# Performance work log

Hardware: AMD Instinct MI355X
Metric: run time of the kernel (lower is better)

The kernel has to match this reference:

```python
import jax, jax.numpy as jnp
import numpy as np

B, S, HID = 2, 2048, 2048
NH = 16
HD = HID // NH  # 128


def setup_inputs() -> dict:
    key = jax.random.key(0)
    ks = jax.random.split(key, 9)
    w = 0.02  # init scale to keep logits in a sane range
    return {
        "hidden_states": jax.random.normal(ks[0], (B, S, HID), dtype=jnp.float32),
        "Wq": jax.random.normal(ks[1], (HID, HID), dtype=jnp.float32) * w,
        "bq": jnp.zeros((HID,), dtype=jnp.float32),
        "Wk": jax.random.normal(ks[2], (HID, HD), dtype=jnp.float32) * w,
        "bk": jnp.zeros((HD,), dtype=jnp.float32),
        "Wv": jax.random.normal(ks[3], (HID, HD), dtype=jnp.float32) * w,
        "bv": jnp.zeros((HD,), dtype=jnp.float32),
        "Wo": jax.random.normal(ks[4], (HID, HID), dtype=jnp.float32) * w,
        "bo": jnp.zeros((HID,), dtype=jnp.float32),
    }


def reference(hidden_states, Wq, bq, Wk, bk, Wv, bv, Wo, bo):
    b, s, _ = hidden_states.shape
    # Projections (weights stored [in, out])
    q = hidden_states @ Wq + bq                      # [B,S,HID]
    k = hidden_states @ Wk + bk                      # [B,S,HD] single shared KV head
    v = hidden_states @ Wv + bv                      # [B,S,HD]
    q = q.reshape(b, s, NH, HD)                      # [B,S,H,D]
    # MQA: all query heads attend to the same K/V
    scores = jnp.einsum("bshd,btd->bhst", q, k) / jnp.sqrt(jnp.float32(HD))  # [B,H,S,S]
    probs = jax.nn.softmax(scores, axis=-1)
    attn = jnp.einsum("bhst,btd->bshd", probs, v)    # [B,S,H,D]
    attn = attn.reshape(b, s, HID)
    return attn @ Wo + bo
```

## Files before the change

### kernel.cpp

```cpp
#include <hip/hip_runtime.h>
#include <math.h>

#define BB  2
#define SS  2048
#define HID 2048
#define NH  16
#define HD  128
#define MT  (BB * SS)
#define NC  (HID + 2 * HD)
#define QK_SCALE 0.08838834764831845f

typedef unsigned short ushort_t;
typedef unsigned int uint_t;
typedef __bf16 bf16x8 __attribute__((ext_vector_type(8)));
typedef short short8 __attribute__((ext_vector_type(8)));
typedef float f32x4 __attribute__((ext_vector_type(4)));

__device__ __forceinline__ ushort_t f2bf(float x) {
    union { float f; uint_t u; } a; a.f = x;
    return (ushort_t)((a.u + 0x7FFFu + ((a.u >> 16) & 1u)) >> 16);
}
__device__ __forceinline__ ushort_t f2bf_fast(float x) {
    union { float f; uint_t u; } a; a.f = x;
    return (ushort_t)((a.u + 0x8000u) >> 16);
}

__device__ __forceinline__ int sw_addr(int r, int c) {
    return ((r >> 1) << 6) + ((((((r & 1) << 2) | c)) ^ ((r >> 1) & 7)) << 3);
}

#define CFENCE() asm volatile("" ::: "memory")

__global__ __launch_bounds__(256) void conv_bf16_kernel(
    const float* __restrict__ in, ushort_t* __restrict__ outb)
{
    const size_t i = ((size_t)blockIdx.x * 256 + threadIdx.x) * 8;
    const float4 a = *(const float4*)&in[i];
    const float4 b = *(const float4*)&in[i + 4];
    short8 o;
    o[0] = (short)f2bf(a.x); o[1] = (short)f2bf(a.y);
    o[2] = (short)f2bf(a.z); o[3] = (short)f2bf(a.w);
    o[4] = (short)f2bf(b.x); o[5] = (short)f2bf(b.y);
    o[6] = (short)f2bf(b.z); o[7] = (short)f2bf(b.w);
    *(short8*)&outb[i] = o;
}

__global__ __launch_bounds__(256) void convT_kernel(
    const float* __restrict__ W, ushort_t* __restrict__ Th, int K, int N)
{
    __shared__ float Ts[64][65];
    const int t = threadIdx.x;
    const int k0 = blockIdx.x * 64, n0 = blockIdx.y * 64;
    const int rr = t >> 4, c4 = (t & 15) * 4;
#pragma unroll
    for (int i = 0; i < 4; i++) {
        const int k = rr + i * 16;
        const float4 v = *(const float4*)&W[(size_t)(k0 + k) * N + n0 + c4];
        Ts[k][c4 + 0] = v.x; Ts[k][c4 + 1] = v.y;
        Ts[k][c4 + 2] = v.z; Ts[k][c4 + 3] = v.w;
    }
    __syncthreads();
    const int n = t >> 2, kc = (t & 3) * 16;
    short8 hv[2];
#pragma unroll
    for (int jj = 0; jj < 16; jj++)
        hv[jj >> 3][jj & 7] = (short)f2bf(Ts[kc + jj][n]);
    const size_t ob = (size_t)(n0 + n) * K + k0 + kc;
    *(short8*)&Th[ob]     = hv[0];
    *(short8*)&Th[ob + 8] = hv[1];
}

__global__ __launch_bounds__(256, 2) void gemm_qkv_kernel(
    const ushort_t* __restrict__ Ab, const ushort_t* __restrict__ WT,
    const float* __restrict__ bq, const float* __restrict__ bk,
    const float* __restrict__ bv,
    ushort_t* __restrict__ qb, ushort_t* __restrict__ kb,
    ushort_t* __restrict__ vtb)
{
    __shared__ short lds[8192];
    constexpr int AH = 0, BH = 4096;
    constexpr int K = HID;
    const int t  = threadIdx.x;
    const int wv = t >> 6, ln = t & 63;
    const int row0 = blockIdx.y * 128, col0 = blockIdx.x * 128;

    size_t agbase[2], bgbase[2];
    int    lbase[2];
#pragma unroll
    for (int i = 0; i < 2; i++) {
        const int I = wv * 2 + i;
        const int lrow = I * 8 + (ln >> 3);
        const int sb = (ln & 7) ^ (lrow & 7);
        const int rr = lrow * 2 + (sb >> 2);
        const int cc = sb & 3;
        agbase[i] = (size_t)(row0 + rr) * K + cc * 8;
        bgbase[i] = (size_t)(col0 + rr) * K + cc * 8;
        lbase[i] = I * 512;
    }

    const int wm0 = (wv & 1) * 64, wn0 = (wv >> 1) * 64;
    const int q = ln >> 4, lm = ln & 15;
    int aoff[4], boff[4];
#pragma unroll
    for (int i = 0; i < 4; i++) aoff[i] = sw_addr(wm0 + i * 16 + lm, q);
#pragma unroll
    for (int j = 0; j < 4; j++) boff[j] = sw_addr(wn0 + j * 16 + lm, q);

    f32x4 acc[4][4];
#pragma unroll
    for (int i = 0; i < 4; i++)
#pragma unroll
        for (int j = 0; j < 4; j++) acc[i][j] = 0.f;

    for (int k0 = 0; k0 < K; k0 += 32) {
        __syncthreads();
#pragma unroll
        for (int i = 0; i < 2; i++) {
            __builtin_amdgcn_global_load_lds(
                (const __attribute__((address_space(1))) void*)(Ab + agbase[i] + k0),
                (__attribute__((address_space(3))) void*)&lds[AH + lbase[i]], 16, 0, 0);
            __builtin_amdgcn_global_load_lds(
                (const __attribute__((address_space(1))) void*)(WT + bgbase[i] + k0),
                (__attribute__((address_space(3))) void*)&lds[BH + lbase[i]], 16, 0, 0);
        }
        __syncthreads();

        bf16x8 ah[4], bh[4];
#pragma unroll
        for (int i = 0; i < 4; i++) ah[i] = *(const bf16x8*)&lds[AH + aoff[i]];
#pragma unroll
        for (int j = 0; j < 4; j++) bh[j] = *(const bf16x8*)&lds[BH + boff[j]];
#pragma unroll
        for (int i = 0; i < 4; i++)
#pragma unroll
            for (int j = 0; j < 4; j++)
                acc[i][j] = __builtin_amdgcn_mfma_f32_16x16x32_bf16(ah[i], bh[j], acc[i][j], 0, 0, 0);
    }

    const int mode = (col0 < HID) ? 0 : ((col0 == HID) ? 1 : 2);
    const float* bsel = (mode == 0) ? bq : ((mode == 1) ? bk : bv);
    const int noff = (mode == 0) ? 0 : ((mode == 1) ? HID : HID + HD);
    float bj[4];
#pragma unroll
    for (int j = 0; j < 4; j++) bj[j] = bsel[col0 - noff + wn0 + j * 16 + lm];
#pragma unroll
    for (int i = 0; i < 4; i++) {
        const int mb = row0 + wm0 + i * 16 + q * 4;
#pragma unroll
        for (int j = 0; j < 4; j++) {
            const int nn = col0 + wn0 + j * 16 + lm;
#pragma unroll
            for (int rr2 = 0; rr2 < 4; rr2++) {
                const float v = acc[i][j][rr2] + bj[j];
                if (mode == 0)      qb [(size_t)(mb + rr2) * HID + nn]           = f2bf_fast(v * QK_SCALE);
                else if (mode == 1) kb [(size_t)(mb + rr2) * HD + (nn - HID)]    = f2bf_fast(v);
                else                vtb[(size_t)(nn - HID - HD) * MT + mb + rr2] = f2bf_fast(v);
            }
        }
    }
}

__global__ __launch_bounds__(256, 2) void gemm_oproj_kernel(
    const ushort_t* __restrict__ Ab, const ushort_t* __restrict__ WT,
    const float* __restrict__ bias, float* __restrict__ C, int M, int N, int K)
{
    __shared__ short lds[8192];
    constexpr int AH = 0, BH = 4096;
    const int t  = threadIdx.x;
    const int wv = t >> 6, ln = t & 63;
    const int row0 = blockIdx.y * 128, col0 = blockIdx.x * 128;

    size_t agbase[2], bgbase[2];
    int    lbase[2];
#pragma unroll
    for (int i = 0; i < 2; i++) {
        const int I = wv * 2 + i;
        const int lrow = I * 8 + (ln >> 3);
        const int sb = (ln & 7) ^ (lrow & 7);
        const int rr = lrow * 2 + (sb >> 2);
        const int cc = sb & 3;
        agbase[i] = (size_t)(row0 + rr) * K + cc * 8;
        bgbase[i] = (size_t)(col0 + rr) * K + cc * 8;
        lbase[i] = I * 512;
    }

    const int wm0 = (wv & 1) * 64, wn0 = (wv >> 1) * 64;
    const int q = ln >> 4, lm = ln & 15;
    int aoff[4], boff[4];
#pragma unroll
    for (int i = 0; i < 4; i++) aoff[i] = sw_addr(wm0 + i * 16 + lm, q);
#pragma unroll
    for (int j = 0; j < 4; j++) boff[j] = sw_addr(wn0 + j * 16 + lm, q);

    f32x4 acc[4][4];
#pragma unroll
    for (int i = 0; i < 4; i++)
#pragma unroll
        for (int j = 0; j < 4; j++) acc[i][j] = 0.f;

    for (int k0 = 0; k0 < K; k0 += 32) {
        __syncthreads();
#pragma unroll
        for (int i = 0; i < 2; i++) {
            __builtin_amdgcn_global_load_lds(
                (const __attribute__((address_space(1))) void*)(Ab + agbase[i] + k0),
                (__attribute__((address_space(3))) void*)&lds[AH + lbase[i]], 16, 0, 0);
            __builtin_amdgcn_global_load_lds(
                (const __attribute__((address_space(1))) void*)(WT + bgbase[i] + k0),
                (__attribute__((address_space(3))) void*)&lds[BH + lbase[i]], 16, 0, 0);
        }
        __syncthreads();

        bf16x8 ah[4], bh[4];
#pragma unroll
        for (int i = 0; i < 4; i++) ah[i] = *(const bf16x8*)&lds[AH + aoff[i]];
#pragma unroll
        for (int j = 0; j < 4; j++) bh[j] = *(const bf16x8*)&lds[BH + boff[j]];
#pragma unroll
        for (int i = 0; i < 4; i++)
#pragma unroll
            for (int j = 0; j < 4; j++)
                acc[i][j] = __builtin_amdgcn_mfma_f32_16x16x32_bf16(ah[i], bh[j], acc[i][j], 0, 0, 0);
    }

    float bj[4];
#pragma unroll
    for (int j = 0; j < 4; j++) bj[j] = bias[col0 + wn0 + j * 16 + lm];
#pragma unroll
    for (int i = 0; i < 4; i++) {
        const int mb = row0 + wm0 + i * 16 + q * 4;
#pragma unroll
        for (int j = 0; j < 4; j++) {
            const int nn = col0 + wn0 + j * 16 + lm;
#pragma unroll
            for (int rr2 = 0; rr2 < 4; rr2++)
                C[(size_t)(mb + rr2) * N + nn] = acc[i][j][rr2] + bj[j];
        }
    }
}

__global__ __launch_bounds__(256, 2) void attn_mfma_kernel(
    const ushort_t* __restrict__ qg, const ushort_t* __restrict__ kg,
    const ushort_t* __restrict__ vtg, ushort_t* Oh)
{
    __shared__ short Ks[2][8192], Vts[2][8192], Ps[4096];
    const int b = blockIdx.z, h = blockIdx.y, qt = blockIdx.x;
    const int t = threadIdx.x, wv = t >> 6, ln = t & 63;
    const int q = ln >> 4, lm = ln & 15;
    const int w16 = wv * 16;
    const int am = w16 + lm, amx = am & 15, amx7 = am & 7;

#pragma unroll
    for (int i = 0; i < 4; i++) {
        const int I = wv * 4 + i;
        const int r = 4 * I + (ln >> 4);
        const int c = (ln & 15) ^ (r & 15);
        const ushort_t* src = qg + (size_t)(b * SS + qt * 64 + r) * HID + h * HD + c * 8;
        __builtin_amdgcn_global_load_lds((const __attribute__((address_space(1))) void*)src,
            (__attribute__((address_space(3))) void*)&Ks[0][I * 512], 16, 0, 0);
    }
    __syncthreads();
    bf16x8 aq[4];
#pragma unroll
    for (int ks = 0; ks < 4; ks++)
        aq[ks] = *(const bf16x8*)&Ks[0][am * 128 + (((ks << 2) | q) ^ amx) * 8];
    __syncthreads();

    size_t kbase[4], vbase[4];
#pragma unroll
    for (int i = 0; i < 4; i++) {
        const int I = wv * 4 + i;
        { const int r = 4 * I + (ln >> 4); const int c = (ln & 15) ^ (r & 15);
          kbase[i] = (size_t)(b * SS + r) * HD + c * 8; }
        { const int r = 8 * I + (ln >> 3); const int c = (ln & 7) ^ (r & 7);
          vbase[i] = (size_t)r * MT + b * SS + c * 8; }
    }

#pragma unroll
    for (int i = 0; i < 4; i++) {
        const int I = wv * 4 + i;
        __builtin_amdgcn_global_load_lds(
            (const __attribute__((address_space(1))) void*)(kg + kbase[i]),
            (__attribute__((address_space(3))) void*)&Ks[0][I * 512], 16, 0, 0);
        __builtin_amdgcn_global_load_lds(
            (const __attribute__((address_space(1))) void*)(vtg + vbase[i]),
            (__attribute__((address_space(3))) void*)&Vts[0][I * 512], 16, 0, 0);
    }

    float lrow[4] = {0.f, 0.f, 0.f, 0.f};
    f32x4 O[8];
#pragma unroll
    for (int ct = 0; ct < 8; ct++) O[ct] = 0.f;

    for (int kt = 0; kt < SS; kt += 64) {
        const int cur = (kt >> 6) & 1;
        const int nxt = cur ^ 1;

        if (kt + 64 < SS) {
#pragma unroll
            for (int i = 0; i < 4; i++) {
                const int I = wv * 4 + i;
                __builtin_amdgcn_global_load_lds(
                    (const __attribute__((address_space(1))) void*)(kg + kbase[i] + (size_t)(kt + 64) * HD),
                    (__attribute__((address_space(3))) void*)&Ks[nxt][I * 512], 16, 0, 0);
                __builtin_amdgcn_global_load_lds(
                    (const __attribute__((address_space(1))) void*)(vtg + vbase[i] + kt + 64),
                    (__attribute__((address_space(3))) void*)&Vts[nxt][I * 512], 16, 0, 0);
            }
            asm volatile("s_waitcnt vmcnt(8)" ::: "memory");
        } else {
            asm volatile("s_waitcnt vmcnt(0)" ::: "memory");
        }
        CFENCE();
        __builtin_amdgcn_s_barrier();
        CFENCE();

        f32x4 s[4];
#pragma unroll
        for (int ct = 0; ct < 4; ct++) s[ct] = 0.f;
        __builtin_amdgcn_s_setprio(1);
#pragma unroll
        for (int ks = 0; ks < 4; ks++) {
#pragma unroll
            for (int ct = 0; ct < 4; ct++) {
                const int n = ct * 16 + lm;
                const bf16x8 bk = *(const bf16x8*)&Ks[cur][n * 128 + (((ks << 2) | q) ^ (n & 15)) * 8];
                s[ct] = __builtin_amdgcn_mfma_f32_16x16x32_bf16(aq[ks], bk, s[ct], 0, 0, 0);
            }
        }
        __builtin_amdgcn_s_setprio(0);

#pragma unroll
        for (int ct = 0; ct < 4; ct++) {
            const int ch = ct * 2 + (lm >> 3);
#pragma unroll
            for (int r = 0; r < 4; r++) {
                const float p = __expf(s[ct][r]);
                lrow[r] += p;
                const int pr = w16 + q * 4 + r;
                Ps[pr * 64 + ((ch ^ (pr & 7)) << 3) + (lm & 7)] = (short)f2bf_fast(p);
            }
        }

        __builtin_amdgcn_s_setprio(1);
#pragma unroll
        for (int ks = 0; ks < 2; ks++) {
            const bf16x8 ap = *(const bf16x8*)&Ps[am * 64 + (((ks << 2) | q) ^ amx7) * 8];
#pragma unroll
            for (int ct = 0; ct < 8; ct++) {
                const int d = ct * 16 + lm;
                const bf16x8 bv = *(const bf16x8*)&Vts[cur][d * 64 + (((ks << 2) | q) ^ (d & 7)) * 8];
                O[ct] = __builtin_amdgcn_mfma_f32_16x16x32_bf16(ap, bv, O[ct], 0, 0, 0);
            }
        }
        __builtin_amdgcn_s_setprio(0);

        CFENCE();
        __builtin_amdgcn_s_barrier();
        CFENCE();
    }

#pragma unroll
    for (int msk = 1; msk < 16; msk <<= 1)
#pragma unroll
        for (int r = 0; r < 4; r++) lrow[r] += __shfl_xor(lrow[r], msk);
#pragma unroll
    for (int r = 0; r < 4; r++) {
        const float inv = 1.f / lrow[r];
        const size_t base = (size_t)(b * SS + qt * 64 + w16 + q * 4 + r) * HID + h * HD;
#pragma unroll
        for (int ct = 0; ct < 8; ct++)
            Oh[base + ct * 16 + lm] = f2bf_fast(O[ct][r] * inv);
    }
}

extern "C" void kernel_launch(void* const* d_in, const int* in_sizes, int n_in,
                              void* d_out, int out_size, void* d_ws, size_t ws_size,
                              hipStream_t stream)
{
    const float* hs = (const float*)d_in[0];
    const float* Wq = (const float*)d_in[1];
    const float* bq = (const float*)d_in[2];
    const float* Wk = (const float*)d_in[3];
    const float* bk = (const float*)d_in[4];
    const float* Wv = (const float*)d_in[5];
    const float* bv = (const float*)d_in[6];
    const float* Wo = (const float*)d_in[7];
    const float* bo = (const float*)d_in[8];
    float* out = (float*)d_out;

    char* w = (char*)d_ws;
    ushort_t* hsb  = (ushort_t*)w;  w += (size_t)MT * HID * 2;
    ushort_t* qb   = (ushort_t*)w;  w += (size_t)MT * HID * 2;
    ushort_t* kb   = (ushort_t*)w;  w += (size_t)MT * HD * 2;
    ushort_t* vtb  = (ushort_t*)w;  w += (size_t)HD * MT * 2;
    ushort_t* WcT  = (ushort_t*)w;  w += (size_t)NC * HID * 2;
    ushort_t* WoT  = WcT;

    conv_bf16_kernel<<<(MT * HID) / (256 * 8), 256, 0, stream>>>(hs, hsb);
    convT_kernel<<<dim3(HID / 64, HID / 64), 256, 0, stream>>>(Wq, WcT, HID, HID);
    convT_kernel<<<dim3(HID / 64, HD / 64),  256, 0, stream>>>(
        Wk, WcT + (size_t)HID * HID, HID, HD);
    convT_kernel<<<dim3(HID / 64, HD / 64),  256, 0, stream>>>(
        Wv, WcT + (size_t)(HID + HD) * HID, HID, HD);

    gemm_qkv_kernel<<<dim3(NC / 128, MT / 128), 256, 0, stream>>>(
        hsb, WcT, bq, bk, bv, qb, kb, vtb);

    convT_kernel<<<dim3(HID / 64, HID / 64), 256, 0, stream>>>(Wo, WoT, HID, HID);

    attn_mfma_kernel<<<dim3(SS / 64, NH, BB), 256, 0, stream>>>(qb, kb, vtb, qb);

    gemm_oproj_kernel<<<dim3(HID / 128, MT / 128), 256, 0, stream>>>(
        qb, WoT, bo, out, MT, HID, HID);
}
```

Before: 337.1 us.

## Single-buffer K/V with staggered prefetch to raise attention occupancy to 4 blocks

Replaces the double-buffered K and V shared-memory tiles with single buffers. The next K tile is now loaded while P·V runs, and the next V tile while the next QK^T runs, with extra barriers and vmcnt waits between stages. LDS per block drops from about 72 KB to 40 KB, and launch bounds are raised to allow 4 blocks per CU for more latency hiding. In exchange there are more barriers per iteration, less slack between each load and its use, and tighter register limits.

```diff
diff --git a/kernel.cpp b/kernel.cpp
--- a/kernel.cpp
+++ b/kernel.cpp
@@ -239,11 +239,11 @@
     }
 }
 
-__global__ __launch_bounds__(256, 2) void attn_mfma_kernel(
+__global__ __launch_bounds__(256, 4) void attn_mfma_kernel(
     const ushort_t* __restrict__ qg, const ushort_t* __restrict__ kg,
     const ushort_t* __restrict__ vtg, ushort_t* Oh)
 {
-    __shared__ short Ks[2][8192], Vts[2][8192], Ps[4096];
+    __shared__ short Ks[8192], Vts[8192], Ps[4096];
     const int b = blockIdx.z, h = blockIdx.y, qt = blockIdx.x;
     const int t = threadIdx.x, wv = t >> 6, ln = t & 63;
     const int q = ln >> 4, lm = ln & 15;
@@ -257,13 +257,13 @@
         const int c = (ln & 15) ^ (r & 15);
         const ushort_t* src = qg + (size_t)(b * SS + qt * 64 + r) * HID + h * HD + c * 8;
         __builtin_amdgcn_global_load_lds((const __attribute__((address_space(1))) void*)src,
-            (__attribute__((address_space(3))) void*)&Ks[0][I * 512], 16, 0, 0);
+            (__attribute__((address_space(3))) void*)&Ks[I * 512], 16, 0, 0);
     }
     __syncthreads();
     bf16x8 aq[4];
 #pragma unroll
     for (int ks = 0; ks < 4; ks++)
-        aq[ks] = *(const bf16x8*)&Ks[0][am * 128 + (((ks << 2) | q) ^ amx) * 8];
+        aq[ks] = *(const bf16x8*)&Ks[am * 128 + (((ks << 2) | q) ^ amx) * 8];
     __syncthreads();
 
     size_t kbase[4], vbase[4];
@@ -281,10 +281,14 @@
         const int I = wv * 4 + i;
         __builtin_amdgcn_global_load_lds(
             (const __attribute__((address_space(1))) void*)(kg + kbase[i]),
-            (__attribute__((address_space(3))) void*)&Ks[0][I * 512], 16, 0, 0);
+            (__attribute__((address_space(3))) void*)&Ks[I * 512], 16, 0, 0);
+    }
+#pragma unroll
+    for (int i = 0; i < 4; i++) {
+        const int I = wv * 4 + i;
         __builtin_amdgcn_global_load_lds(
             (const __attribute__((address_space(1))) void*)(vtg + vbase[i]),
-            (__attribute__((address_space(3))) void*)&Vts[0][I * 512], 16, 0, 0);
+            (__attribute__((address_space(3))) void*)&Vts[I * 512], 16, 0, 0);
     }
 
     float lrow[4] = {0.f, 0.f, 0.f, 0.f};
@@ -293,42 +297,40 @@
     for (int ct = 0; ct < 8; ct++) O[ct] = 0.f;
 
     for (int kt = 0; kt < SS; kt += 64) {
-        const int cur = (kt >> 6) & 1;
-        const int nxt = cur ^ 1;
-
-        if (kt + 64 < SS) {
+        const int more = (kt + 64 < SS);
+
+        asm volatile("s_waitcnt vmcnt(4)" ::: "memory");
+        CFENCE();
+        __builtin_amdgcn_s_barrier();
+        CFENCE();
+
+        f32x4 s[4];
+#pragma unroll
+        for (int ct = 0; ct < 4; ct++) s[ct] = 0.f;
+        __builtin_amdgcn_s_setprio(1);
+#pragma unroll
+        for (int ks = 0; ks < 4; ks++) {
+#pragma unroll
+            for (int ct = 0; ct < 4; ct++) {
+                const int n = ct * 16 + lm;
+                const bf16x8 bk = *(const bf16x8*)&Ks[n * 128 + (((ks << 2) | q) ^ (n & 15)) * 8];
+                s[ct] = __builtin_amdgcn_mfma_f32_16x16x32_bf16(aq[ks], bk, s[ct], 0, 0, 0);
+            }
+        }
+        __builtin_amdgcn_s_setprio(0);
+
+        CFENCE();
+        __builtin_amdgcn_s_barrier();
+        CFENCE();
+        if (more) {
 #pragma unroll
             for (int i = 0; i < 4; i++) {
                 const int I = wv * 4 + i;
                 __builtin_amdgcn_global_load_lds(
                     (const __attribute__((address_space(1))) void*)(kg + kbase[i] + (size_t)(kt + 64) * HD),
-                    (__attribute__((address_space(3))) void*)&Ks[nxt][I * 512], 16, 0, 0);
-                __builtin_amdgcn_global_load_lds(
-                    (const __attribute__((address_space(1))) void*)(vtg + vbase[i] + kt + 64),
-                    (__attribute__((address_space(3))) void*)&Vts[nxt][I * 512], 16, 0, 0);
-            }
-            asm volatile("s_waitcnt vmcnt(8)" ::: "memory");
-        } else {
-            asm volatile("s_waitcnt vmcnt(0)" ::: "memory");
-        }
-        CFENCE();
-        __builtin_amdgcn_s_barrier();
-        CFENCE();
-
-        f32x4 s[4];
-#pragma unroll
-        for (int ct = 0; ct < 4; ct++) s[ct] = 0.f;
-        __builtin_amdgcn_s_setprio(1);
-#pragma unroll
-        for (int ks = 0; ks < 4; ks++) {
-#pragma unroll
-            for (int ct = 0; ct < 4; ct++) {
-                const int n = ct * 16 + lm;
-                const bf16x8 bk = *(const bf16x8*)&Ks[cur][n * 128 + (((ks << 2) | q) ^ (n & 15)) * 8];
-                s[ct] = __builtin_amdgcn_mfma_f32_16x16x32_bf16(aq[ks], bk, s[ct], 0, 0, 0);
-            }
-        }
-        __builtin_amdgcn_s_setprio(0);
+                    (__attribute__((address_space(3))) void*)&Ks[I * 512], 16, 0, 0);
+            }
+        }
 
 #pragma unroll
         for (int ct = 0; ct < 4; ct++) {
@@ -342,6 +344,12 @@
             }
         }
 
+        if (more) asm volatile("s_waitcnt vmcnt(4)" ::: "memory");
+        else      asm volatile("s_waitcnt vmcnt(0)" ::: "memory");
+        CFENCE();
+        __builtin_amdgcn_s_barrier();
+        CFENCE();
+
         __builtin_amdgcn_s_setprio(1);
 #pragma unroll
         for (int ks = 0; ks < 2; ks++) {
@@ -349,7 +357,7 @@
 #pragma unroll
             for (int ct = 0; ct < 8; ct++) {
                 const int d = ct * 16 + lm;
-                const bf16x8 bv = *(const bf16x8*)&Vts[cur][d * 64 + (((ks << 2) | q) ^ (d & 7)) * 8];
+                const bf16x8 bv = *(const bf16x8*)&Vts[d * 64 + (((ks << 2) | q) ^ (d & 7)) * 8];
                 O[ct] = __builtin_amdgcn_mfma_f32_16x16x32_bf16(ap, bv, O[ct], 0, 0, 0);
             }
         }
@@ -358,6 +366,15 @@
         CFENCE();
         __builtin_amdgcn_s_barrier();
         CFENCE();
+        if (more) {
+#pragma unroll
+            for (int i = 0; i < 4; i++) {
+                const int I = wv * 4 + i;
+                __builtin_amdgcn_global_load_lds(
+                    (const __attribute__((address_space(1))) void*)(vtg + vbase[i] + kt + 64),
+                    (__attribute__((address_space(3))) void*)&Vts[I * 512], 16, 0, 0);
+            }
+        }
     }
 
 #pragma unroll
```

After: 324.9 us. 1.04x faster.
